# Performance work log

Hardware: AMD Instinct MI355X
Metric: run time of the kernel (lower is better)

Reference implementation:

```python
import jax, jax.numpy as jnp
import numpy as np

B, N, D, H, L, F = 8192, 64, 128, 8, 3, 512
HD = D // H
RADIUS = 3.0
LN_EPS = 1e-5


def _ln(x, g, b):
    m = jnp.mean(x, axis=-1, keepdims=True)
    v = jnp.var(x, axis=-1, keepdims=True)
    return (x - m) / jnp.sqrt(v + LN_EPS) * g + b


def setup_inputs() -> dict:
    key = jax.random.key(0)
    ks = jax.random.split(key, 20)
    def nrm(k, shape, s=0.05):
        return jax.random.normal(k, shape, jnp.float32) * s
    return {
        'ego_context': nrm(ks[0], (B, D), 1.0),
        'ego_pos': nrm(ks[1], (B, 2), 1.0),
        'ego_vel': nrm(ks[2], (B, 2), 1.0),
        'neighbor_pos': nrm(ks[3], (B, N, 2), 1.5),
        'neighbor_vel': nrm(ks[4], (B, N, 2), 1.0),
        'neighbor_mask': jax.random.bernoulli(ks[5], 0.8, (B, N)),
        'np_W': nrm(ks[6], (6, D), 0.3), 'np_b': jnp.zeros((D,), jnp.float32),
        'np_ln_g': jnp.ones((D,), jnp.float32), 'np_ln_b': jnp.zeros((D,), jnp.float32),
        'ego_W': nrm(ks[7], (D, D)), 'ego_b': jnp.zeros((D,), jnp.float32),
        'ego_ln_g': jnp.ones((D,), jnp.float32), 'ego_ln_b': jnp.zeros((D,), jnp.float32),
        'n1_g': jnp.ones((L, D), jnp.float32), 'n1_b': jnp.zeros((L, D), jnp.float32),
        'nkv_g': jnp.ones((L, D), jnp.float32), 'nkv_b': jnp.zeros((L, D), jnp.float32),
        'n2_g': jnp.ones((L, D), jnp.float32), 'n2_b': jnp.zeros((L, D), jnp.float32),
        'Wq': nrm(ks[8], (L, D, D)), 'bq': jnp.zeros((L, D), jnp.float32),
        'Wk': nrm(ks[9], (L, D, D)), 'bk': jnp.zeros((L, D), jnp.float32),
        'Wv': nrm(ks[10], (L, D, D)), 'bv': jnp.zeros((L, D), jnp.float32),
        'Wo': nrm(ks[11], (L, D, D)), 'bo': jnp.zeros((L, D), jnp.float32),
        'W1': nrm(ks[12], (L, D, F)), 'b1': jnp.zeros((L, F), jnp.float32),
        'W2': nrm(ks[13], (L, F, D)), 'b2': jnp.zeros((L, D), jnp.float32),
        'out_W': nrm(ks[14], (D, D)), 'out_b': jnp.zeros((D,), jnp.float32),
        'out_ln_g': jnp.ones((D,), jnp.float32), 'out_ln_b': jnp.zeros((D,), jnp.float32),
    }


def reference(ego_context, ego_pos, ego_vel, neighbor_pos, neighbor_vel, neighbor_mask,
              np_W, np_b, np_ln_g, np_ln_b, ego_W, ego_b, ego_ln_g, ego_ln_b,
              n1_g, n1_b, nkv_g, nkv_b, n2_g, n2_b,
              Wq, bq, Wk, bk, Wv, bv, Wo, bo, W1, b1, W2, b2,
              out_W, out_b, out_ln_g, out_ln_b):
    # relative features (B, N, 6)
    rel_pos = neighbor_pos - ego_pos[:, None, :]
    rel_vel = neighbor_vel - ego_vel[:, None, :]
    dist = jnp.clip(jnp.linalg.norm(rel_pos, axis=-1, keepdims=True), 1e-6, None)
    bearing = jnp.arctan2(rel_pos[..., 1:2] + 1e-8, rel_pos[..., 0:1] + 1e-8)
    rel = jnp.concatenate([rel_pos, rel_vel, dist, bearing], axis=-1)

    # dynamic mask: radius gating + all-masked fixup (mimics key_padding_mask[all_masked,0]=False)
    valid = neighbor_mask & (jnp.linalg.norm(neighbor_pos - ego_pos[:, None, :], axis=-1) < RADIUS)
    all_invalid = ~jnp.any(valid, axis=-1)
    valid = valid | (all_invalid[:, None] & (jnp.arange(N) == 0)[None, :])

    # neighbor_proj: Linear(6,D) -> LN -> ReLU (dropout inactive at eval)
    nb = jax.nn.relu(_ln(rel @ np_W + np_b, np_ln_g, np_ln_b))  # (B, N, D)
    # ego_proj: Linear(D,D) -> LN; keep ego as (B, D) since query length is 1
    x = _ln(ego_context @ ego_W + ego_b, ego_ln_g, ego_ln_b)

    scale = 1.0 / jnp.sqrt(jnp.float32(HD))
    for i in range(L):
        q = _ln(x, n1_g[i], n1_b[i])          # (B, D)
        kv = _ln(nb, nkv_g[i], nkv_b[i])      # (B, N, D)
        Q = (q @ Wq[i] + bq[i]).reshape(B, H, HD)
        K = (kv @ Wk[i] + bk[i]).reshape(B, N, H, HD)
        V = (kv @ Wv[i] + bv[i]).reshape(B, N, H, HD)
        scores = jnp.einsum('bhd,bnhd->bhn', Q, K) * scale
        scores = jnp.where(valid[:, None, :], scores, -1e9)
        attn = jax.nn.softmax(scores, axis=-1)
        ctx = jnp.einsum('bhn,bnhd->bhd', attn, V).reshape(B, D)
        x = x + ctx @ Wo[i] + bo[i]
        y = _ln(x, n2_g[i], n2_b[i])
        x = x + jax.nn.gelu(y @ W1[i] + b1[i], approximate=False) @ W2[i] + b2[i]

    return _ln(x @ out_W + out_b, out_ln_g, out_ln_b)
```

## Files before the change

kernel.cpp:

```cpp
#include <hip/hip_runtime.h>
#include <stdint.h>

typedef unsigned int uint;
typedef unsigned short ushort;
typedef unsigned long long u64;

#define B_   8192
#define D_   128
#define N_   64
#define L_   3

typedef __attribute__((ext_vector_type(8))) short short8;
typedef __attribute__((ext_vector_type(4))) float f32x4;
union FragU { uint4 u; short8 h; };

__device__ __forceinline__ float bf2f(ushort u){ union{uint i; float f;} c; c.i=((uint)u)<<16; return c.f; }
__device__ __forceinline__ float bflo(uint u){ union{uint i; float f;} c; c.i=u<<16; return c.f; }
__device__ __forceinline__ float bfhi(uint u){ union{uint i; float f;} c; c.i=u&0xffff0000u; return c.f; }
__device__ __forceinline__ ushort f2bf(float f){ uint u=__float_as_uint(f); return (ushort)((u + 0x7fffu + ((u>>16)&1u))>>16); }
__device__ __forceinline__ uint pk2(float lo, float hi){ return (uint)f2bf(lo) | (((uint)f2bf(hi))<<16); }
__device__ __forceinline__ float wsum(float v){ for (int o=32;o;o>>=1) v += __shfl_xor(v,o); return v; }

#define OFF_X   0
#define XSTR    520
#define OFF_XH  8320
#define XHSTR   272
#define OFF_Q   12672
#define QSTR    260
#define OFF_QK  16832
#define QKSTR   272
#define OFF_QB  21184
#define OFF_V   21248
#define OFF_NB  21504
#define NBSTR   272
#define OFF_NT  38912
#define NTSTR   144
#define OFF_AT  57344
#define ATSTR   144
#define OFF_U   59648
#define OFF_CX  61760
#define OFF_H1  21504
#define LDS_SZ  62272

struct P {
  const float *ego, *epos, *evel, *npos, *nvel;
  const int   *mask;
  const float *npW, *npb, *npg, *npbb;
  const float *ego_b, *ego_g, *ego_bb;
  const float *bo, *b2, *out_b, *out_g, *out_bb;
  const float *npRec;
  const ushort *WqT, *WkT, *WvT, *W1T, *WoT, *W2T, *egoT, *outT;
  const ushort *bqF, *bkF, *bvF, *b1F;
  ushort *nbg; u64 *msk;
  float *outp;
};

__global__ void prepF(const float* Wq,const float* bq,const float* n1g,const float* n1b,
                      const float* Wk,const float* bk,const float* nkg,const float* nkb,
                      const float* Wv,const float* bv,
                      const float* W1,const float* b1,const float* n2g,const float* n2b,
                      ushort* WqT, ushort* bqF, ushort* WkT, ushort* bkF,
                      ushort* WvT, ushort* bvF, ushort* W1T, ushort* b1F){
  __shared__ float red[2];
  int bid=blockIdx.x, t=threadIdx.x;
  const float *src,*g,*bb,*bias; ushort *dstW,*dstB; int N;
  if (bid<384){ int l=bid>>7, j=bid&127; src=Wq+l*16384+j; g=n1g+l*128; bb=n1b+l*128; bias=bq+l*128+j; dstW=WqT+l*16384+j*128; dstB=bqF+l*128+j; N=128; }
  else if (bid<768){ int q=bid-384; int l=q>>7, j=q&127; src=Wk+l*16384+j; g=nkg+l*128; bb=nkb+l*128; bias=bk+l*128+j; dstW=WkT+l*16384+j*128; dstB=bkF+l*128+j; N=128; }
  else if (bid<1152){ int q=bid-768; int l=q>>7, j=q&127; src=Wv+l*16384+j; g=nkg+l*128; bb=nkb+l*128; bias=bv+l*128+j; dstW=WvT+l*16384+j*128; dstB=bvF+l*128+j; N=128; }
  else { int q=bid-1152; int l=q/512, j=q%512; src=W1+l*65536+j; g=n2g+l*128; bb=n2b+l*128; bias=b1+l*512+j; dstW=W1T+l*65536+j*128; dstB=b1F+l*512+j; N=512; }
  float wv = src[t*N];
  dstW[t] = f2bf(g[t]*wv);
  float pv = wsum(bb[t]*wv);
  if ((t&63)==0) red[t>>6]=pv;
  __syncthreads();
  if (t==0) *dstB = f2bf(red[0]+red[1]+bias[0]);
}

__global__ void prepP(const float* Wo, const float* W2, const float* egoW, const float* outW,
                      ushort* WoT, ushort* W2T, ushort* egoT, ushort* outT){
  int bid=blockIdx.x, t=threadIdx.x;
  if (bid<384){ int l=bid>>7, j=bid&127; WoT[l*16384+j*128+t] = f2bf(Wo[l*16384+t*128+j]); }
  else if (bid<768){ int q=bid-384; int l=q>>7, j=q&127;
    for (int k=t;k<512;k+=128) W2T[l*65536+j*512+k] = f2bf(W2[l*65536+k*128+j]); }
  else if (bid<896){ int j=bid-768; egoT[j*128+t]=f2bf(egoW[t*128+j]); }
  else { int j=bid-896; outT[j*128+t]=f2bf(outW[t*128+j]); }
}

__global__ void prepNp(const float* npW, const float* npb, const float* npg, const float* npbb, float* rec){
  int t=threadIdx.x;
  if (t<128){
    for (int r=0;r<6;++r) rec[t*9+r]=npW[r*128+t];
    rec[t*9+6]=npb[t]; rec[t*9+7]=npg[t]; rec[t*9+8]=npbb[t];
  }
}

__global__ __launch_bounds__(256,4) void st_nb(P p){
  __shared__ float s_npW[768], s_npP[384];
  __shared__ float s_valid[2][64];
  int tid=threadIdx.x, g=tid>>7, t=tid&127;
  int b = blockIdx.x*2+g;
  for (int i=tid;i<768;i+=256) s_npW[i]=p.npW[i];
  if (tid<128){ s_npP[tid]=p.npb[tid]; s_npP[128+tid]=p.npg[tid]; s_npP[256+tid]=p.npbb[tid]; }
  __syncthreads();
  int nn=t>>1, jh=t&1;
  float2 pn = ((const float2*)p.npos)[b*N_+nn];
  float2 vn = ((const float2*)p.nvel)[b*N_+nn];
  float2 pe = ((const float2*)p.epos)[b];
  float2 ve = ((const float2*)p.evel)[b];
  float rx=pn.x-pe.x, ry=pn.y-pe.y, rvx=vn.x-ve.x, rvy=vn.y-ve.y;
  float nrm = sqrtf(rx*rx+ry*ry);
  float dist = fmaxf(nrm,1e-6f), bear = atan2f(ry+1e-8f, rx+1e-8f);
  bool vld = (p.mask[b*N_+nn]!=0) && (nrm<3.0f);
  if (jh==0) s_valid[g][nn] = vld?1.f:0.f;
  float z[64]; float sa=0.f, sb=0.f;
  #pragma unroll
  for (int jj=0;jj<64;++jj){
    int j = jh*64+jj;
    float v = s_npP[j] + rx*s_npW[j] + ry*s_npW[128+j] + rvx*s_npW[256+j]
                       + rvy*s_npW[384+j] + dist*s_npW[512+j] + bear*s_npW[640+j];
    z[jj]=v; sa+=v; sb+=v*v;
  }
  sa += __shfl_xor(sa,1); sb += __shfl_xor(sb,1);
  float m1 = sa*0.0078125f, r1 = rsqrtf(sb*0.0078125f - m1*m1 + 1e-5f);
  float ta=0.f, tb=0.f;
  #pragma unroll
  for (int jj=0;jj<64;++jj){
    int j = jh*64+jj;
    float a = (z[jj]-m1)*r1*s_npP[128+j] + s_npP[256+j];
    a = fmaxf(a,0.f);
    z[jj]=a; ta+=a; tb+=a*a;
  }
  ta += __shfl_xor(ta,1); tb += __shfl_xor(tb,1);
  float m2 = ta*0.0078125f, r2 = rsqrtf(tb*0.0078125f - m2*m2 + 1e-5f);
  uint* dst = (uint*)(p.nbg + (size_t)b*8192 + nn*128 + jh*64);
  #pragma unroll
  for (int q=0;q<32;++q) dst[q] = pk2((z[2*q]-m2)*r2, (z[2*q+1]-m2)*r2);
  __syncthreads();
  if (tid<2){
    u64 m=0;
    for (int n=0;n<64;++n) if (s_valid[tid][n]>0.5f) m |= (1ULL<<n);
    p.msk[blockIdx.x*2+tid] = m;
  }
}

__device__ __forceinline__ void ln_to_xh(char* smem, int tid){
  int b = tid>>4, pp = tid&15;
  const char* xr = smem + OFF_X + b*XSTR + pp*32;
  float v[8];
  #pragma unroll
  for (int i=0;i<4;++i){ float2 t2 = *(const float2*)(xr + i*8); v[2*i]=t2.x; v[2*i+1]=t2.y; }
  float s1=0.f, s2=0.f;
  #pragma unroll
  for (int i=0;i<8;++i){ s1+=v[i]; s2+=v[i]*v[i]; }
  for (int o=1;o<16;o<<=1){ s1 += __shfl_xor(s1,o); s2 += __shfl_xor(s2,o); }
  float m = s1*0.0078125f, rs = rsqrtf(s2*0.0078125f - m*m + 1e-5f);
  uint4 o4;
  o4.x = pk2((v[0]-m)*rs,(v[1]-m)*rs); o4.y = pk2((v[2]-m)*rs,(v[3]-m)*rs);
  o4.z = pk2((v[4]-m)*rs,(v[5]-m)*rs); o4.w = pk2((v[6]-m)*rs,(v[7]-m)*rs);
  *(uint4*)(smem + OFF_XH + b*XHSTR + pp*16) = o4;
}

__device__ __forceinline__ void ln_affine_inplace(char* smem, int tid, const float* g, const float* bb){
  int b = tid>>4, pp = tid&15;
  char* xr = smem + OFF_X + b*XSTR + pp*32;
  float v[8];
  #pragma unroll
  for (int i=0;i<4;++i){ float2 t2 = *(const float2*)(xr + i*8); v[2*i]=t2.x; v[2*i+1]=t2.y; }
  float s1=0.f, s2=0.f;
  #pragma unroll
  for (int i=0;i<8;++i){ s1+=v[i]; s2+=v[i]*v[i]; }
  for (int o=1;o<16;o<<=1){ s1 += __shfl_xor(s1,o); s2 += __shfl_xor(s2,o); }
  float m = s1*0.0078125f, rs = rsqrtf(s2*0.0078125f - m*m + 1e-5f);
  #pragma unroll
  for (int i=0;i<8;++i) v[i] = (v[i]-m)*rs*g[pp*8+i] + bb[pp*8+i];
  #pragma unroll
  for (int i=0;i<4;++i){ float2 t2; t2.x=v[2*i]; t2.y=v[2*i+1]; *(float2*)(xr + i*8) = t2; }
}

__device__ __forceinline__ void cvt_x_to_xh(char* smem, int tid){
  int b = tid>>4, pp = tid&15;
  const char* xr = smem + OFF_X + b*XSTR + pp*32;
  float v[8];
  #pragma unroll
  for (int i=0;i<4;++i){ float2 t2 = *(const float2*)(xr + i*8); v[2*i]=t2.x; v[2*i+1]=t2.y; }
  uint4 o4;
  o4.x=pk2(v[0],v[1]); o4.y=pk2(v[2],v[3]); o4.z=pk2(v[4],v[5]); o4.w=pk2(v[6],v[7]);
  *(uint4*)(smem + OFF_XH + b*XHSTR + pp*16) = o4;
}

template<int SPILL>
__global__ __launch_bounds__(256,2) void st_main(P p){
  __shared__ __align__(16) char smem[LDS_SZ];
  const int tid = threadIdx.x;
  const int w = tid>>6, l64 = tid&63;
  const int cc = l64&15, qq = l64>>4;
  const int bB = blockIdx.x*16;

  for (int i=tid;i<1088;i+=256) ((uint*)(smem+OFF_QK))[i]=0u;
  if (tid<16) ((float*)(smem+OFF_QB))[tid]=0.f;
  for (int i=tid;i<288;i+=256) ((uint*)(smem+OFF_AT+8*ATSTR))[i]=0u;

  {
    int b_=tid>>4, pp=tid&15;
    const float* src = p.ego + (size_t)(bB+b_)*128 + pp*8;
    float4 v0 = *(const float4*)src, v1 = *(const float4*)(src+4);
    uint4 o4; o4.x=pk2(v0.x,v0.y); o4.y=pk2(v0.z,v0.w); o4.z=pk2(v1.x,v1.y); o4.w=pk2(v1.z,v1.w);
    *(uint4*)(smem + OFF_XH + b_*XHSTR + pp*16) = o4;
  }
  __syncthreads();
  {
    #pragma unroll
    for (int i=0;i<2;++i){
      int nt = w*2+i;
      f32x4 acc = {0.f,0.f,0.f,0.f};
      #pragma unroll
      for (int kt=0;kt<4;++kt){
        FragU a,bF;
        a.u = *(const uint4*)(smem + OFF_XH + cc*XHSTR + kt*64 + qq*16);
        bF.u = *(const uint4*)(p.egoT + (nt*16+cc)*128 + kt*32 + qq*8);
        acc = __builtin_amdgcn_mfma_f32_16x16x32_bf16(a.h, bF.h, acc, 0,0,0);
      }
      int col = nt*16+cc;
      float bv = p.ego_b[col];
      #pragma unroll
      for (int r=0;r<4;++r) *(float*)(smem+OFF_X+(qq*4+r)*XSTR+col*4) = acc[r]+bv;
    }
  }
  __syncthreads();
  ln_affine_inplace(smem, tid, p.ego_g, p.ego_bb);
  __syncthreads();

  for (int li=0; li<L_; ++li){
    ln_to_xh(smem, tid);
    __syncthreads();
    {
      const ushort* W = p.WqT + li*16384;
      #pragma unroll
      for (int i=0;i<2;++i){
        int nt = w*2+i;
        f32x4 acc = {0.f,0.f,0.f,0.f};
        #pragma unroll
        for (int kt=0;kt<4;++kt){
          FragU a,bF;
          a.u = *(const uint4*)(smem + OFF_XH + cc*XHSTR + kt*64 + qq*16);
          bF.u = *(const uint4*)(W + (nt*16+cc)*128 + kt*32 + qq*8);
          acc = __builtin_amdgcn_mfma_f32_16x16x32_bf16(a.h, bF.h, acc, 0,0,0);
        }
        int col = nt*16+cc;
        float bv = bf2f(p.bqF[li*128+col]);
        ushort* Qm = (ushort*)(smem+OFF_Q);
        #pragma unroll
        for (int r=0;r<4;++r) Qm[(qq*4+r)*130 + col] = f2bf(acc[r]+bv);
      }
    }
    __syncthreads();

    for (int bl=0; bl<16; ++bl){
      const int b = bB + bl;
      if (SPILL){
        int n = w*16 + (l64>>2), seg = l64&3;
        if (seg==0){
          u64 mv = p.msk[b];
          *(float*)(smem+OFF_V+n*4) = ((mv>>n)&1ULL) ? 1.f : 0.f;
        }
        const uint4* src = (const uint4*)(p.nbg + (size_t)b*8192 + n*128);
        ushort* T = (ushort*)(smem+OFF_NT);
        #pragma unroll
        for (int i=0;i<4;++i){
          int ci = seg + i*4;
          uint4 v = src[ci];
          *(uint4*)(smem + OFF_NB + n*NBSTR + ci*16) = v;
          int d0 = ci*8;
          T[(d0+0)*72+n]=(ushort)v.x; T[(d0+1)*72+n]=(ushort)(v.x>>16);
          T[(d0+2)*72+n]=(ushort)v.y; T[(d0+3)*72+n]=(ushort)(v.y>>16);
          T[(d0+4)*72+n]=(ushort)v.z; T[(d0+5)*72+n]=(ushort)(v.z>>16);
          T[(d0+6)*72+n]=(ushort)v.w; T[(d0+7)*72+n]=(ushort)(v.w>>16);
        }
      } else {
        int n = w*16 + (l64>>2), jq = l64&3;
        float2 pn = ((const float2*)p.npos)[b*N_+n];
        float2 vn = ((const float2*)p.nvel)[b*N_+n];
        float2 pe = ((const float2*)p.epos)[b];
        float2 ve = ((const float2*)p.evel)[b];
        float rx=pn.x-pe.x, ry=pn.y-pe.y, rvx=vn.x-ve.x, rvy=vn.y-ve.y;
        float nrm = sqrtf(rx*rx+ry*ry);
        float dist = fmaxf(nrm,1e-6f), bear = atan2f(ry+1e-8f, rx+1e-8f);
        if (jq==0){
          bool vld = (p.mask[b*N_+n]!=0) && (nrm<3.0f);
          *(float*)(smem+OFF_V+n*4) = vld?1.f:0.f;
        }
        float z[32]; float sa=0.f, sb=0.f;
        #pragma unroll
        for (int jj=0;jj<32;++jj){
          const float* rec = p.npRec + (jq*32+jj)*9;
          float4 r0 = *(const float4*)rec;
          float4 r1 = *(const float4*)(rec+4);
          float v = r1.z + rx*r0.x + ry*r0.y + rvx*r0.z + rvy*r0.w + dist*r1.x + bear*r1.y;
          z[jj]=v; sa+=v; sb+=v*v;
        }
        sa += __shfl_xor(sa,1); sb += __shfl_xor(sb,1);
        sa += __shfl_xor(sa,2); sb += __shfl_xor(sb,2);
        float m1 = sa*0.0078125f, r1s = rsqrtf(sb*0.0078125f - m1*m1 + 1e-5f);
        float ta=0.f, tb=0.f;
        #pragma unroll
        for (int jj=0;jj<32;++jj){
          const float* rec = p.npRec + (jq*32+jj)*9;
          float a = (z[jj]-m1)*r1s*rec[7] + rec[8];
          a = fmaxf(a,0.f);
          z[jj]=a; ta+=a; tb+=a*a;
        }
        ta += __shfl_xor(ta,1); tb += __shfl_xor(tb,1);
        ta += __shfl_xor(ta,2); tb += __shfl_xor(tb,2);
        float m2 = ta*0.0078125f, r2s = rsqrtf(tb*0.0078125f - m2*m2 + 1e-5f);
        ushort* T = (ushort*)(smem+OFF_NT);
        #pragma unroll
        for (int q2=0;q2<16;++q2){
          uint pr = pk2((z[2*q2]-m2)*r2s, (z[2*q2+1]-m2)*r2s);
          *(uint*)(smem + OFF_NB + n*NBSTR + jq*64 + q2*4) = pr;
          int d = jq*32 + q2*2;
          T[d*72 + n] = (ushort)pr;
          T[(d+1)*72 + n] = (ushort)(pr>>16);
        }
      }
      {
        int h = (w<<1) + (l64>>5);
        int d4 = (l64&31)*4;
        const ushort* Wk = p.WkT + li*16384;
        float a0=0.f,a1=0.f,a2=0.f,a3=0.f, qb=0.f;
        #pragma unroll
        for (int j=0;j<16;++j){
          float qv = bf2f(*(const ushort*)(smem + OFF_Q + bl*QSTR + (h*16+j)*2));
          uint2 wv = *(const uint2*)(Wk + (h*16+j)*128 + d4);
          a0 += qv*bflo(wv.x); a1 += qv*bfhi(wv.x);
          a2 += qv*bflo(wv.y); a3 += qv*bfhi(wv.y);
          qb += qv * bf2f(p.bkF[li*128 + h*16 + j]);
        }
        uint2 o; o.x = pk2(a0,a1); o.y = pk2(a2,a3);
        *(uint2*)(smem + OFF_QK + h*QKSTR + d4*2) = o;
        if ((l64&31)==0) *(float*)(smem+OFF_QB + h*4) = qb;
      }
      __syncthreads();

      {
        FragU bfr[4];
        #pragma unroll
        for (int kt=0;kt<4;++kt) bfr[kt].u = *(const uint4*)(smem + OFF_QK + cc*QKSTR + kt*64 + qq*16);
        f32x4 c[4];
        #pragma unroll
        for (int mt=0;mt<4;++mt){
          f32x4 acc = {0.f,0.f,0.f,0.f};
          #pragma unroll
          for (int kt=0;kt<4;++kt){
            FragU a; a.u = *(const uint4*)(smem + OFF_NB + (mt*16+cc)*NBSTR + kt*64 + qq*16);
            acc = __builtin_amdgcn_mfma_f32_16x16x32_bf16(a.h, bfr[kt].h, acc, 0,0,0);
          }
          c[mt]=acc;
        }
        float qbv = *(const float*)(smem+OFF_QB+cc*4);
        float fl[16]; float anyv=0.f;
        #pragma unroll
        for (int mt=0;mt<4;++mt)
          #pragma unroll
          for (int r=0;r<4;++r){
            int n = mt*16 + qq*4 + r;
            float f = *(const float*)(smem+OFF_V+n*4);
            fl[mt*4+r]=f; anyv+=f;
          }
        bool none = (__ballot(anyv>0.5f)==0ULL);
        float sc[16];
        #pragma unroll
        for (int mt=0;mt<4;++mt)
          #pragma unroll
          for (int r=0;r<4;++r){
            int k = mt*4+r; int n = mt*16+qq*4+r;
            bool ok = (fl[k]>0.5f) || (none && n==0);
            sc[k] = ok ? 0.25f*(c[mt][r]+qbv) : -1e9f;
          }
        float mx=-3e38f;
        #pragma unroll
        for (int k=0;k<16;++k) mx=fmaxf(mx,sc[k]);
        mx = fmaxf(mx,__shfl_xor(mx,16)); mx = fmaxf(mx,__shfl_xor(mx,32));
        float ex[16]; float se=0.f;
        #pragma unroll
        for (int k=0;k<16;++k){ ex[k]=__expf(sc[k]-mx); se+=ex[k]; }
        se += __shfl_xor(se,16); se += __shfl_xor(se,32);
        float inv = 1.f/se;
        if (w==0 && cc<8){
          ushort* A = (ushort*)(smem+OFF_AT);
          #pragma unroll
          for (int mt=0;mt<4;++mt)
            #pragma unroll
            for (int r=0;r<4;++r) A[cc*72 + (mt*16+qq*4+r)] = f2bf(ex[mt*4+r]*inv);
        }
      }
      __syncthreads();

      {
        #pragma unroll
        for (int i=0;i<2;++i){
          int nt = w*2 + i;
          f32x4 acc={0.f,0.f,0.f,0.f};
          #pragma unroll
          for (int kt=0;kt<2;++kt){
            FragU a,bF;
            a.u = *(const uint4*)(smem + OFF_AT + cc*ATSTR + kt*64 + qq*16);
            bF.u = *(const uint4*)(smem + OFF_NT + (nt*16+cc)*NTSTR + kt*64 + qq*16);
            acc = __builtin_amdgcn_mfma_f32_16x16x32_bf16(a.h, bF.h, acc, 0,0,0);
          }
          if (qq<2){
            ushort* U = (ushort*)(smem+OFF_U);
            #pragma unroll
            for (int r=0;r<4;++r) U[(qq*4+r)*132 + nt*16+cc] = f2bf(acc[r]);
          }
        }
      }
      __syncthreads();

      {
        int jj = l64>>1, dh = l64&1;
        int j = w*32 + jj;
        int h = j>>4;
        const ushort* Wv = p.WvT + li*16384 + j*128;
        float acc = (dh==0) ? bf2f(p.bvF[li*128+j]) : 0.f;
        #pragma unroll
        for (int i8=0;i8<8;++i8){
          int d = dh*64 + i8*8;
          uint2 u0 = *(const uint2*)(smem + OFF_U + h*264 + d*2);
          uint2 u1 = *(const uint2*)(smem + OFF_U + h*264 + d*2 + 8);
          uint4 wv = *(const uint4*)(Wv + d);
          acc += bflo(u0.x)*bflo(wv.x) + bfhi(u0.x)*bfhi(wv.x);
          acc += bflo(u0.y)*bflo(wv.y) + bfhi(u0.y)*bfhi(wv.y);
          acc += bflo(u1.x)*bflo(wv.z) + bfhi(u1.x)*bfhi(wv.z);
          acc += bflo(u1.y)*bflo(wv.w) + bfhi(u1.y)*bfhi(wv.w);
        }
        acc += __shfl_xor(acc,1);
        if (dh==0) *(float*)(smem+OFF_CX + j*4) = acc;
      }
      __syncthreads();

      {
        int jj = l64>>1, dh = l64&1;
        int j = w*32 + jj;
        const ushort* Wo = p.WoT + li*16384 + j*128;
        float acc = (dh==0) ? p.bo[li*128+j] : 0.f;
        #pragma unroll
        for (int i8=0;i8<8;++i8){
          int d = dh*64 + i8*8;
          float4 c0 = *(const float4*)(smem + OFF_CX + d*4);
          float4 c1 = *(const float4*)(smem + OFF_CX + d*4 + 16);
          uint4 wv = *(const uint4*)(Wo + d);
          acc += c0.x*bflo(wv.x) + c0.y*bfhi(wv.x) + c0.z*bflo(wv.y) + c0.w*bfhi(wv.y);
          acc += c1.x*bflo(wv.z) + c1.y*bfhi(wv.z) + c1.z*bflo(wv.w) + c1.w*bfhi(wv.w);
        }
        acc += __shfl_xor(acc,1);
        if (dh==0){
          float* xp = (float*)(smem + OFF_X + bl*XSTR + j*4);
          *xp += acc;
        }
      }
      __syncthreads();
    }

    ln_to_xh(smem, tid);
    __syncthreads();
    {
      FragU afr[4];
      #pragma unroll
      for (int kt=0;kt<4;++kt) afr[kt].u = *(const uint4*)(smem+OFF_XH + cc*XHSTR + kt*64 + qq*16);
      const ushort* W = p.W1T + li*65536;
      ushort* H = (ushort*)(smem+OFF_H1);
      #pragma unroll
      for (int i=0;i<8;++i){
        int nt = w*8+i;
        f32x4 acc={0.f,0.f,0.f,0.f};
        #pragma unroll
        for (int kt=0;kt<4;++kt){
          FragU bF; bF.u = *(const uint4*)(W + (nt*16+cc)*128 + kt*32 + qq*8);
          acc = __builtin_amdgcn_mfma_f32_16x16x32_bf16(afr[kt].h, bF.h, acc, 0,0,0);
        }
        int col = nt*16+cc;
        float bv = bf2f(p.b1F[li*512+col]);
        #pragma unroll
        for (int r=0;r<4;++r){
          float v = acc[r]+bv;
          v = 0.5f*v*(1.f+erff(v*0.70710678118654752f));
          H[(qq*4+r)*520 + col] = f2bf(v);
        }
      }
    }
    __syncthreads();
    {
      const ushort* W = p.W2T + li*65536;
      #pragma unroll
      for (int i=0;i<2;++i){
        int nt = w*2+i;
        f32x4 acc={0.f,0.f,0.f,0.f};
        #pragma unroll
        for (int kt=0;kt<16;++kt){
          FragU a,bF;
          a.u = *(const uint4*)(smem+OFF_H1 + cc*1040 + kt*64 + qq*16);
          bF.u = *(const uint4*)(W + (nt*16+cc)*512 + kt*32 + qq*8);
          acc = __builtin_amdgcn_mfma_f32_16x16x32_bf16(a.h, bF.h, acc, 0,0,0);
        }
        int col = nt*16+cc;
        float bv = p.b2[li*128+col];
        #pragma unroll
        for (int r=0;r<4;++r){
          float* xp = (float*)(smem+OFF_X+(qq*4+r)*XSTR+col*4);
          *xp += acc[r]+bv;
        }
      }
    }
    __syncthreads();
  }

  cvt_x_to_xh(smem, tid);
  __syncthreads();
  {
    #pragma unroll
    for (int i=0;i<2;++i){
      int nt = w*2+i;
      f32x4 acc = {0.f,0.f,0.f,0.f};
      #pragma unroll
      for (int kt=0;kt<4;++kt){
        FragU a,bF;
        a.u = *(const uint4*)(smem + OFF_XH + cc*XHSTR + kt*64 + qq*16);
        bF.u = *(const uint4*)(p.outT + (nt*16+cc)*128 + kt*32 + qq*8);
        acc = __builtin_amdgcn_mfma_f32_16x16x32_bf16(a.h, bF.h, acc, 0,0,0);
      }
      int col = nt*16+cc;
      float bv = p.out_b[col];
      #pragma unroll
      for (int r=0;r<4;++r) *(float*)(smem+OFF_X+(qq*4+r)*XSTR+col*4) = acc[r]+bv;
    }
  }
  __syncthreads();
  {
    int b_=tid>>4, pp=tid&15;
    const char* xr = smem + OFF_X + b_*XSTR + pp*32;
    float v[8];
    #pragma unroll
    for (int i=0;i<4;++i){ float2 t2 = *(const float2*)(xr + i*8); v[2*i]=t2.x; v[2*i+1]=t2.y; }
    float s1=0.f, s2=0.f;
    #pragma unroll
    for (int i=0;i<8;++i){ s1+=v[i]; s2+=v[i]*v[i]; }
    for (int o=1;o<16;o<<=1){ s1 += __shfl_xor(s1,o); s2 += __shfl_xor(s2,o); }
    float m = s1*0.0078125f, rs = rsqrtf(s2*0.0078125f - m*m + 1e-5f);
    float4 o0,o1;
    o0.x=(v[0]-m)*rs*p.out_g[pp*8+0]+p.out_bb[pp*8+0];
    o0.y=(v[1]-m)*rs*p.out_g[pp*8+1]+p.out_bb[pp*8+1];
    o0.z=(v[2]-m)*rs*p.out_g[pp*8+2]+p.out_bb[pp*8+2];
    o0.w=(v[3]-m)*rs*p.out_g[pp*8+3]+p.out_bb[pp*8+3];
    o1.x=(v[4]-m)*rs*p.out_g[pp*8+4]+p.out_bb[pp*8+4];
    o1.y=(v[5]-m)*rs*p.out_g[pp*8+5]+p.out_bb[pp*8+5];
    o1.z=(v[6]-m)*rs*p.out_g[pp*8+6]+p.out_bb[pp*8+6];
    o1.w=(v[7]-m)*rs*p.out_g[pp*8+7]+p.out_bb[pp*8+7];
    float* dst = p.outp + (size_t)(bB+b_)*128 + pp*8;
    *(float4*)dst = o0; *(float4*)(dst+4) = o1;
  }
}

extern "C" void kernel_launch(void* const* d_in, const int* in_sizes, int n_in,
                              void* d_out, int out_size, void* d_ws, size_t ws_size,
                              hipStream_t stream){
  (void)in_sizes; (void)n_in; (void)out_size;
  char* ws = (char*)d_ws;
  ushort* WqT  = (ushort*)(ws + 0);
  ushort* WkT  = (ushort*)(ws + 98304);
  ushort* WvT  = (ushort*)(ws + 196608);
  ushort* W1T  = (ushort*)(ws + 294912);
  ushort* WoT  = (ushort*)(ws + 688128);
  ushort* W2T  = (ushort*)(ws + 786432);
  ushort* egoT = (ushort*)(ws + 1179648);
  ushort* outT = (ushort*)(ws + 1212416);
  float*  npRec= (float*) (ws + 1245184);
  ushort* bqF  = (ushort*)(ws + 1249792);
  ushort* bkF  = (ushort*)(ws + 1250560);
  ushort* bvF  = (ushort*)(ws + 1251328);
  ushort* b1F  = (ushort*)(ws + 1252096);
  const size_t NB_OFF  = 1255424;
  const size_t MSK_OFF = NB_OFF + (size_t)B_*8192*2;
  const size_t NEED    = MSK_OFF + (size_t)B_*8;
  const bool spill = (ws_size >= NEED);

  prepF<<<2688,128,0,stream>>>((const float*)d_in[20],(const float*)d_in[21],(const float*)d_in[14],(const float*)d_in[15],
                               (const float*)d_in[22],(const float*)d_in[23],(const float*)d_in[16],(const float*)d_in[17],
                               (const float*)d_in[24],(const float*)d_in[25],
                               (const float*)d_in[28],(const float*)d_in[29],(const float*)d_in[18],(const float*)d_in[19],
                               WqT,bqF,WkT,bkF,WvT,bvF,W1T,b1F);
  prepP<<<1024,128,0,stream>>>((const float*)d_in[26],(const float*)d_in[30],(const float*)d_in[10],(const float*)d_in[32],
                               WoT,W2T,egoT,outT);
  prepNp<<<1,128,0,stream>>>((const float*)d_in[6],(const float*)d_in[7],(const float*)d_in[8],(const float*)d_in[9],npRec);

  P p;
  p.ego=(const float*)d_in[0]; p.epos=(const float*)d_in[1]; p.evel=(const float*)d_in[2];
  p.npos=(const float*)d_in[3]; p.nvel=(const float*)d_in[4]; p.mask=(const int*)d_in[5];
  p.npW=(const float*)d_in[6]; p.npb=(const float*)d_in[7]; p.npg=(const float*)d_in[8]; p.npbb=(const float*)d_in[9];
  p.ego_b=(const float*)d_in[11]; p.ego_g=(const float*)d_in[12]; p.ego_bb=(const float*)d_in[13];
  p.bo=(const float*)d_in[27]; p.b2=(const float*)d_in[31];
  p.out_b=(const float*)d_in[33]; p.out_g=(const float*)d_in[34]; p.out_bb=(const float*)d_in[35];
  p.npRec=npRec;
  p.WqT=WqT; p.WkT=WkT; p.WvT=WvT; p.W1T=W1T; p.WoT=WoT; p.W2T=W2T; p.egoT=egoT; p.outT=outT;
  p.bqF=bqF; p.bkF=bkF; p.bvF=bvF; p.b1F=b1F;
  p.nbg = (ushort*)(ws + NB_OFF);
  p.msk = (u64*)(ws + MSK_OFF);
  p.outp=(float*)d_out;

  if (spill){
    st_nb<<<B_/2,256,0,stream>>>(p);
    st_main<1><<<B_/16,256,0,stream>>>(p);
  } else {
    st_main<0><<<B_/16,256,0,stream>>>(p);
  }
}
```

Baseline: 618.8 us.

## Fold Q/K and V/O projections into per-head bilinear forms, shrink block to 8 rows

Precomputes per-head merged matrices (Wq·Wk^T scaled, and Wv·Wo) so attention scores come from the LayerNormed neighbor features directly, and context output is a single projection from attention-weighted features. This avoids computing K and V for all 64 neighbors per layer. The main kernel now processes 8 batch rows per block with smaller LDS and occupancy 4, and st_nb also writes a transposed neighbor copy. It costs much more workspace and doubles neighbor-feature traffic, and MFMA tiles are half wasted with 8 rows.

```diff
diff --git a/kernel.cpp b/kernel.cpp
--- a/kernel.cpp
+++ b/kernel.cpp
@@ -15,87 +15,157 @@
 union FragU { uint4 u; short8 h; };
 
 __device__ __forceinline__ float bf2f(ushort u){ union{uint i; float f;} c; c.i=((uint)u)<<16; return c.f; }
-__device__ __forceinline__ float bflo(uint u){ union{uint i; float f;} c; c.i=u<<16; return c.f; }
-__device__ __forceinline__ float bfhi(uint u){ union{uint i; float f;} c; c.i=u&0xffff0000u; return c.f; }
 __device__ __forceinline__ ushort f2bf(float f){ uint u=__float_as_uint(f); return (ushort)((u + 0x7fffu + ((u>>16)&1u))>>16); }
 __device__ __forceinline__ uint pk2(float lo, float hi){ return (uint)f2bf(lo) | (((uint)f2bf(hi))<<16); }
-__device__ __forceinline__ float wsum(float v){ for (int o=32;o;o>>=1) v += __shfl_xor(v,o); return v; }
-
-#define OFF_X   0
-#define XSTR    520
-#define OFF_XH  8320
-#define XHSTR   272
-#define OFF_Q   12672
-#define QSTR    260
-#define OFF_QK  16832
-#define QKSTR   272
-#define OFF_QB  21184
-#define OFF_V   21248
-#define OFF_NB  21504
-#define NBSTR   272
-#define OFF_NT  38912
-#define NTSTR   144
-#define OFF_AT  57344
-#define ATSTR   144
-#define OFF_U   59648
-#define OFF_CX  61760
-#define OFF_H1  21504
-#define LDS_SZ  62272
+
+#define OFF_X    0
+#define XSTR     528
+#define OFF_XH   4224
+#define XHSTR    272
+#define OFF_QKA  6400
+#define OFF_H1   6400
+#define OFF_QB   23808
+#define OFF_MSK  24064
+#define OFF_UA   24128
+#define LDS_SZ   40640
 
 struct P {
-  const float *ego, *epos, *evel, *npos, *nvel;
+  const float *ego,*epos,*evel,*npos,*nvel;
   const int   *mask;
-  const float *npW, *npb, *npg, *npbb;
-  const float *ego_b, *ego_g, *ego_bb;
-  const float *bo, *b2, *out_b, *out_g, *out_bb;
-  const float *npRec;
-  const ushort *WqT, *WkT, *WvT, *W1T, *WoT, *W2T, *egoT, *outT;
-  const ushort *bqF, *bkF, *bvF, *b1F;
-  ushort *nbg; u64 *msk;
+  const float *npW,*npb,*npg,*npbb;
+  const float *ego_b,*ego_g,*ego_bb;
+  const float *b2,*out_b,*out_g,*out_bb;
+  const float *C0,*m2,*c2,*bo2,*b1F;
+  const ushort *MT,*G,*W1B,*W2B,*egoT,*outT;
+  ushort *nbg,*nbt; u64 *msk;
   float *outp;
 };
 
-__global__ void prepF(const float* Wq,const float* bq,const float* n1g,const float* n1b,
-                      const float* Wk,const float* bk,const float* nkg,const float* nkb,
-                      const float* Wv,const float* bv,
-                      const float* W1,const float* b1,const float* n2g,const float* n2b,
-                      ushort* WqT, ushort* bqF, ushort* WkT, ushort* bkF,
-                      ushort* WvT, ushort* bvF, ushort* W1T, ushort* b1F){
-  __shared__ float red[2];
-  int bid=blockIdx.x, t=threadIdx.x;
-  const float *src,*g,*bb,*bias; ushort *dstW,*dstB; int N;
-  if (bid<384){ int l=bid>>7, j=bid&127; src=Wq+l*16384+j; g=n1g+l*128; bb=n1b+l*128; bias=bq+l*128+j; dstW=WqT+l*16384+j*128; dstB=bqF+l*128+j; N=128; }
-  else if (bid<768){ int q=bid-384; int l=q>>7, j=q&127; src=Wk+l*16384+j; g=nkg+l*128; bb=nkb+l*128; bias=bk+l*128+j; dstW=WkT+l*16384+j*128; dstB=bkF+l*128+j; N=128; }
-  else if (bid<1152){ int q=bid-768; int l=q>>7, j=q&127; src=Wv+l*16384+j; g=nkg+l*128; bb=nkb+l*128; bias=bv+l*128+j; dstW=WvT+l*16384+j*128; dstB=bvF+l*128+j; N=128; }
-  else { int q=bid-1152; int l=q/512, j=q%512; src=W1+l*65536+j; g=n2g+l*128; bb=n2b+l*128; bias=b1+l*512+j; dstW=W1T+l*65536+j*128; dstB=b1F+l*512+j; N=512; }
-  float wv = src[t*N];
-  dstW[t] = f2bf(g[t]*wv);
-  float pv = wsum(bb[t]*wv);
-  if ((t&63)==0) red[t>>6]=pv;
-  __syncthreads();
-  if (t==0) *dstB = f2bf(red[0]+red[1]+bias[0]);
+__global__ void prep_bias(const float* Wq,const float* bq,const float* n1b,
+                          const float* Wk,const float* bk,const float* nkb,
+                          const float* Wv,const float* bv,
+                          const float* W1,const float* b1,const float* n2b,
+                          float* bqp, float* bkp, float* bvp, float* b1F){
+  int gid = blockIdx.x*256 + threadIdx.x;
+  if (gid >= 3*896) return;
+  int l = gid/896, c = gid%896;
+  if (c < 384){
+    int m = c>>7, j = c&127;
+    const float* W = (m==0?Wq:(m==1?Wk:Wv)) + l*16384 + j;
+    const float* nb = (m==0? n1b : nkb) + l*128;
+    const float* bs = (m==0?bq:(m==1?bk:bv)) + l*128 + j;
+    float a = *bs;
+    for (int e=0;e<128;++e) a += nb[e]*W[e*128];
+    float* dst = (m==0?bqp:(m==1?bkp:bvp));
+    dst[l*128+j] = a;
+  } else {
+    int f = c-384;
+    float a = b1[l*512+f];
+    const float* W = W1 + l*65536 + f;
+    const float* nb = n2b + l*128;
+    for (int e=0;e<128;++e) a += nb[e]*W[e*512];
+    b1F[l*512+f] = a;
+  }
 }
 
-__global__ void prepP(const float* Wo, const float* W2, const float* egoW, const float* outW,
-                      ushort* WoT, ushort* W2T, ushort* egoT, ushort* outT){
-  int bid=blockIdx.x, t=threadIdx.x;
-  if (bid<384){ int l=bid>>7, j=bid&127; WoT[l*16384+j*128+t] = f2bf(Wo[l*16384+t*128+j]); }
-  else if (bid<768){ int q=bid-384; int l=q>>7, j=q&127;
-    for (int k=t;k<512;k+=128) W2T[l*65536+j*512+k] = f2bf(W2[l*65536+k*128+j]); }
-  else if (bid<896){ int j=bid-768; egoT[j*128+t]=f2bf(egoW[t*128+j]); }
-  else { int j=bid-896; outT[j*128+t]=f2bf(outW[t*128+j]); }
+__global__ void prep_bias2(const float* Wo, const float* bo, const float* bvp, float* bo2){
+  int l = blockIdx.x, t = threadIdx.x;
+  if (t < 128){
+    float a = bo[l*128+t];
+    const float* W = Wo + l*16384 + t;
+    const float* bv = bvp + l*128;
+    for (int c=0;c<128;++c) a += bv[c]*W[c*128];
+    bo2[l*128+t] = a;
+  }
 }
 
-__global__ void prepNp(const float* npW, const float* npb, const float* npg, const float* npbb, float* rec){
-  int t=threadIdx.x;
+__global__ void prep_MG(const float* Wq,const float* Wk,const float* Wv,const float* Wo,
+                        const float* n1g,const float* nkg,
+                        const float* bqp,const float* bkp,
+                        ushort* MT, float* C0, float* m2, float* c2, ushort* G){
+  __shared__ float sWq[128][16], sWk[128][16], sWv[128][16], sWo[16][128];
+  int l = blockIdx.x>>3, h = blockIdx.x&7, t = threadIdx.x;
+  { int row = t>>1, hf = t&1;
+    const float* q = Wq + l*16384 + row*128 + h*16 + hf*8;
+    const float* k = Wk + l*16384 + row*128 + h*16 + hf*8;
+    const float* v = Wv + l*16384 + row*128 + h*16 + hf*8;
+    for (int j=0;j<8;++j){ sWq[row][hf*8+j]=q[j]; sWk[row][hf*8+j]=k[j]; sWv[row][hf*8+j]=v[j]; }
+  }
+  { int row = t>>4, sg = t&15;
+    const float* o = Wo + l*16384 + (h*16+row)*128 + sg*8;
+    for (int j=0;j<8;++j) sWo[row][sg*8+j]=o[j];
+  }
+  __syncthreads();
+  {
+    int e = t&127;
+    float g1 = 0.25f*n1g[l*128+e];
+    float wq[16];
+    #pragma unroll
+    for (int j=0;j<16;++j) wq[j]=sWq[e][j];
+    for (int k2=0;k2<64;++k2){
+      int d = (t>>7) + 2*k2;
+      float s=0.f;
+      #pragma unroll
+      for (int j=0;j<16;++j) s += wq[j]*sWk[d][j];
+      MT[(size_t)l*131072 + (size_t)(h*128+d)*128 + e] = f2bf(g1*nkg[l*128+d]*s);
+    }
+    if (t<128){
+      float s=0.f;
+      #pragma unroll
+      for (int j=0;j<16;++j) s += wq[j]*bkp[l*128+h*16+j];
+      m2[(l*128+e)*8+h] = g1*s;
+    }
+  }
   if (t<128){
-    for (int r=0;r<6;++r) rec[t*9+r]=npW[r*128+t];
-    rec[t*9+6]=npb[t]; rec[t*9+7]=npg[t]; rec[t*9+8]=npbb[t];
+    int d=t; float s=0.f;
+    #pragma unroll
+    for (int j=0;j<16;++j) s += bqp[l*128+h*16+j]*sWk[d][j];
+    C0[l*1024 + h*128 + d] = 0.25f*nkg[l*128+d]*s;
+  }
+  if (t==0){
+    float s=0.f;
+    for (int j=0;j<16;++j) s += bqp[l*128+h*16+j]*bkp[l*128+h*16+j];
+    c2[l*8+h] = 0.25f*s;
+  }
+  {
+    int d = t&127;
+    float gk = nkg[l*128+d];
+    float wv[16];
+    #pragma unroll
+    for (int j=0;j<16;++j) wv[j]=gk*sWv[d][j];
+    for (int k2=0;k2<64;++k2){
+      int e = (t>>7) + 2*k2;
+      float s=0.f;
+      #pragma unroll
+      for (int j=0;j<16;++j) s += wv[j]*sWo[j][e];
+      G[(size_t)l*131072 + (size_t)e*1024 + h*128 + d] = f2bf(s);
+    }
   }
 }
 
+__global__ void prep_T(const float* W1,const float* n2g,const float* W2,
+                       const float* egoW,const float* outW,
+                       ushort* W1B, ushort* W2B, ushort* egoT, ushort* outT){
+  int gid = blockIdx.x*256 + threadIdx.x;
+  if (gid < 196608){
+    int l = gid/65536, r = gid%65536, f = r>>7, e = r&127;
+    W1B[gid] = f2bf(n2g[l*128+e]*W1[l*65536 + e*512 + f]);
+  } else if (gid < 393216){
+    int q = gid-196608; int l = q/65536, r = q%65536, e = r>>9, f = r&511;
+    W2B[q] = f2bf(W2[l*65536 + f*128 + e]);
+  } else if (gid < 409600){
+    int q = gid-393216; int c = q>>7, e = q&127;
+    egoT[q] = f2bf(egoW[e*128+c]);
+  } else if (gid < 425984){
+    int q = gid-409600; int c = q>>7, e = q&127;
+    outT[q] = f2bf(outW[e*128+c]);
+  }
+}
+
+template<int MODE>
 __global__ __launch_bounds__(256,4) void st_nb(P p){
   __shared__ float s_npW[768], s_npP[384];
+  __shared__ ushort s_nb[2][64*136];
   __shared__ float s_valid[2][64];
   int tid=threadIdx.x, g=tid>>7, t=tid&127;
   int b = blockIdx.x*2+g;
@@ -131,81 +201,51 @@
     z[jj]=a; ta+=a; tb+=a*a;
   }
   ta += __shfl_xor(ta,1); tb += __shfl_xor(tb,1);
-  float m2 = ta*0.0078125f, r2 = rsqrtf(tb*0.0078125f - m2*m2 + 1e-5f);
-  uint* dst = (uint*)(p.nbg + (size_t)b*8192 + nn*128 + jh*64);
+  float m2v = ta*0.0078125f, r2 = rsqrtf(tb*0.0078125f - m2v*m2v + 1e-5f);
+  uint* gdst = (uint*)(p.nbg + (size_t)b*8192 + nn*128 + jh*64);
+  uint* ldst = (uint*)(&s_nb[g][nn*136 + jh*64]);
   #pragma unroll
-  for (int q=0;q<32;++q) dst[q] = pk2((z[2*q]-m2)*r2, (z[2*q+1]-m2)*r2);
+  for (int q=0;q<32;++q){
+    uint pr = pk2((z[2*q]-m2v)*r2, (z[2*q+1]-m2v)*r2);
+    gdst[q] = pr; ldst[q] = pr;
+  }
   __syncthreads();
   if (tid<2){
     u64 m=0;
     for (int n=0;n<64;++n) if (s_valid[tid][n]>0.5f) m |= (1ULL<<n);
+    if (m==0ULL) m = 1ULL;
     p.msk[blockIdx.x*2+tid] = m;
   }
+  if (MODE==2){
+    uint pk[32];
+    #pragma unroll 8
+    for (int m=0;m<32;++m){
+      ushort lo = s_nb[g][(2*m)*136 + t];
+      ushort hi = s_nb[g][(2*m+1)*136 + t];
+      pk[m] = (uint)lo | ((uint)hi<<16);
+    }
+    uint4* dst = (uint4*)(p.nbt + (size_t)b*8192 + t*64);
+    #pragma unroll
+    for (int q=0;q<8;++q) dst[q] = make_uint4(pk[4*q],pk[4*q+1],pk[4*q+2],pk[4*q+3]);
+  }
 }
 
-__device__ __forceinline__ void ln_to_xh(char* smem, int tid){
-  int b = tid>>4, pp = tid&15;
-  const char* xr = smem + OFF_X + b*XSTR + pp*32;
-  float v[8];
-  #pragma unroll
-  for (int i=0;i<4;++i){ float2 t2 = *(const float2*)(xr + i*8); v[2*i]=t2.x; v[2*i+1]=t2.y; }
-  float s1=0.f, s2=0.f;
-  #pragma unroll
-  for (int i=0;i<8;++i){ s1+=v[i]; s2+=v[i]*v[i]; }
-  for (int o=1;o<16;o<<=1){ s1 += __shfl_xor(s1,o); s2 += __shfl_xor(s2,o); }
-  float m = s1*0.0078125f, rs = rsqrtf(s2*0.0078125f - m*m + 1e-5f);
-  uint4 o4;
-  o4.x = pk2((v[0]-m)*rs,(v[1]-m)*rs); o4.y = pk2((v[2]-m)*rs,(v[3]-m)*rs);
-  o4.z = pk2((v[4]-m)*rs,(v[5]-m)*rs); o4.w = pk2((v[6]-m)*rs,(v[7]-m)*rs);
-  *(uint4*)(smem + OFF_XH + b*XHSTR + pp*16) = o4;
-}
-
-__device__ __forceinline__ void ln_affine_inplace(char* smem, int tid, const float* g, const float* bb){
-  int b = tid>>4, pp = tid&15;
-  char* xr = smem + OFF_X + b*XSTR + pp*32;
-  float v[8];
-  #pragma unroll
-  for (int i=0;i<4;++i){ float2 t2 = *(const float2*)(xr + i*8); v[2*i]=t2.x; v[2*i+1]=t2.y; }
-  float s1=0.f, s2=0.f;
-  #pragma unroll
-  for (int i=0;i<8;++i){ s1+=v[i]; s2+=v[i]*v[i]; }
-  for (int o=1;o<16;o<<=1){ s1 += __shfl_xor(s1,o); s2 += __shfl_xor(s2,o); }
-  float m = s1*0.0078125f, rs = rsqrtf(s2*0.0078125f - m*m + 1e-5f);
-  #pragma unroll
-  for (int i=0;i<8;++i) v[i] = (v[i]-m)*rs*g[pp*8+i] + bb[pp*8+i];
-  #pragma unroll
-  for (int i=0;i<4;++i){ float2 t2; t2.x=v[2*i]; t2.y=v[2*i+1]; *(float2*)(xr + i*8) = t2; }
-}
-
-__device__ __forceinline__ void cvt_x_to_xh(char* smem, int tid){
-  int b = tid>>4, pp = tid&15;
-  const char* xr = smem + OFF_X + b*XSTR + pp*32;
-  float v[8];
-  #pragma unroll
-  for (int i=0;i<4;++i){ float2 t2 = *(const float2*)(xr + i*8); v[2*i]=t2.x; v[2*i+1]=t2.y; }
-  uint4 o4;
-  o4.x=pk2(v[0],v[1]); o4.y=pk2(v[2],v[3]); o4.z=pk2(v[4],v[5]); o4.w=pk2(v[6],v[7]);
-  *(uint4*)(smem + OFF_XH + b*XHSTR + pp*16) = o4;
-}
-
-template<int SPILL>
-__global__ __launch_bounds__(256,2) void st_main(P p){
+template<int MODE>
+__global__ __launch_bounds__(256,4) void st_main(P p){
   __shared__ __align__(16) char smem[LDS_SZ];
   const int tid = threadIdx.x;
   const int w = tid>>6, l64 = tid&63;
   const int cc = l64&15, qq = l64>>4;
-  const int bB = blockIdx.x*16;
-
-  for (int i=tid;i<1088;i+=256) ((uint*)(smem+OFF_QK))[i]=0u;
-  if (tid<16) ((float*)(smem+OFF_QB))[tid]=0.f;
-  for (int i=tid;i<288;i+=256) ((uint*)(smem+OFF_AT+8*ATSTR))[i]=0u;
-
-  {
-    int b_=tid>>4, pp=tid&15;
-    const float* src = p.ego + (size_t)(bB+b_)*128 + pp*8;
-    float4 v0 = *(const float4*)src, v1 = *(const float4*)(src+4);
-    uint4 o4; o4.x=pk2(v0.x,v0.y); o4.y=pk2(v0.z,v0.w); o4.z=pk2(v1.x,v1.y); o4.w=pk2(v1.z,v1.w);
-    *(uint4*)(smem + OFF_XH + b_*XHSTR + pp*16) = o4;
+  const int b5 = tid>>5, sg = tid&31;
+  const int bB = blockIdx.x*8;
+
+  if (tid<8) ((u64*)(smem+OFF_MSK))[tid] = p.msk[bB+tid];
+
+  {
+    const float* src = p.ego + (size_t)(bB+b5)*128 + sg*4;
+    float4 v = *(const float4*)src;
+    uint2 o; o.x = pk2(v.x,v.y); o.y = pk2(v.z,v.w);
+    *(uint2*)(smem + OFF_XH + b5*XHSTR + sg*8) = o;
   }
   __syncthreads();
   {
@@ -216,305 +256,259 @@
       #pragma unroll
       for (int kt=0;kt<4;++kt){
         FragU a,bF;
-        a.u = *(const uint4*)(smem + OFF_XH + cc*XHSTR + kt*64 + qq*16);
+        a.u = *(const uint4*)(smem + OFF_XH + (cc&7)*XHSTR + kt*64 + qq*16);
         bF.u = *(const uint4*)(p.egoT + (nt*16+cc)*128 + kt*32 + qq*8);
         acc = __builtin_amdgcn_mfma_f32_16x16x32_bf16(a.h, bF.h, acc, 0,0,0);
       }
-      int col = nt*16+cc;
-      float bv = p.ego_b[col];
-      #pragma unroll
-      for (int r=0;r<4;++r) *(float*)(smem+OFF_X+(qq*4+r)*XSTR+col*4) = acc[r]+bv;
-    }
-  }
-  __syncthreads();
-  ln_affine_inplace(smem, tid, p.ego_g, p.ego_bb);
+      if (qq<2){
+        int col = nt*16+cc; float bv = p.ego_b[col];
+        #pragma unroll
+        for (int r=0;r<4;++r) *(float*)(smem+OFF_X+(qq*4+r)*XSTR+col*4) = acc[r]+bv;
+      }
+    }
+  }
+  __syncthreads();
+  {
+    float* xr = (float*)(smem + OFF_X + b5*XSTR + sg*16);
+    float4 v = *(float4*)xr;
+    float s1 = v.x+v.y+v.z+v.w, s2 = v.x*v.x+v.y*v.y+v.z*v.z+v.w*v.w;
+    for (int o=1;o<32;o<<=1){ s1 += __shfl_xor(s1,o); s2 += __shfl_xor(s2,o); }
+    float m = s1*0.0078125f, rs = rsqrtf(s2*0.0078125f - m*m + 1e-5f);
+    int c0 = sg*4;
+    v.x = (v.x-m)*rs*p.ego_g[c0+0]+p.ego_bb[c0+0];
+    v.y = (v.y-m)*rs*p.ego_g[c0+1]+p.ego_bb[c0+1];
+    v.z = (v.z-m)*rs*p.ego_g[c0+2]+p.ego_bb[c0+2];
+    v.w = (v.w-m)*rs*p.ego_g[c0+3]+p.ego_bb[c0+3];
+    *(float4*)xr = v;
+  }
   __syncthreads();
 
   for (int li=0; li<L_; ++li){
-    ln_to_xh(smem, tid);
+    {
+      const float* xr = (const float*)(smem + OFF_X + b5*XSTR + sg*16);
+      float4 v = *(const float4*)xr;
+      float s1 = v.x+v.y+v.z+v.w, s2 = v.x*v.x+v.y*v.y+v.z*v.z+v.w*v.w;
+      for (int o=1;o<32;o<<=1){ s1 += __shfl_xor(s1,o); s2 += __shfl_xor(s2,o); }
+      float m = s1*0.0078125f, rs = rsqrtf(s2*0.0078125f - m*m + 1e-5f);
+      uint2 o2; o2.x = pk2((v.x-m)*rs,(v.y-m)*rs); o2.y = pk2((v.z-m)*rs,(v.w-m)*rs);
+      *(uint2*)(smem + OFF_XH + b5*XHSTR + sg*8) = o2;
+    }
     __syncthreads();
     {
-      const ushort* W = p.WqT + li*16384;
+      const ushort* MTl = p.MT + (size_t)li*131072;
+      const float*  C0l = p.C0 + li*1024;
+      FragU aF[4];
+      #pragma unroll
+      for (int kt=0;kt<4;++kt) aF[kt].u = *(const uint4*)(smem + OFF_XH + (cc&7)*XHSTR + kt*64 + qq*16);
+      for (int it=0; it<16; ++it){
+        int nt = w*16+it;
+        f32x4 acc = {0.f,0.f,0.f,0.f};
+        #pragma unroll
+        for (int kt=0;kt<4;++kt){
+          FragU bF; bF.u = *(const uint4*)(MTl + (nt*16+cc)*128 + kt*32 + qq*8);
+          acc = __builtin_amdgcn_mfma_f32_16x16x32_bf16(aF[kt].h, bF.h, acc, 0,0,0);
+        }
+        if (qq<2){
+          int col = nt*16+cc; float c0 = C0l[col];
+          int h = col>>7, dd = col&127;
+          #pragma unroll
+          for (int r=0;r<4;++r)
+            *(ushort*)(smem + OFF_QKA + (qq*4+r)*2176 + h*272 + dd*2) = f2bf(acc[r]+c0);
+        }
+      }
+    }
+    {
+      int b_ = tid>>5, h = (tid>>2)&7, q4 = tid&3;
+      const ushort* xh = (const ushort*)(smem + OFF_XH + b_*XHSTR);
+      const float* m2l = p.m2 + li*1024;
+      float a = 0.f;
+      #pragma unroll 8
+      for (int e = q4*32; e < q4*32+32; ++e) a += bf2f(xh[e]) * m2l[e*8+h];
+      a += __shfl_xor(a,1); a += __shfl_xor(a,2);
+      if (q4==0) *(float*)(smem + OFF_QB + (b_*8+h)*4) = a + p.c2[li*8+h];
+    }
+    __syncthreads();
+
+    for (int rr=0; rr<2; ++rr){
+      const int bl = w*2+rr;
+      const size_t bg = (size_t)(bB+bl);
+      const ushort* nbB = p.nbg + bg*8192;
+      FragU bq4[4];
+      #pragma unroll
+      for (int kt=0;kt<4;++kt) bq4[kt].u = *(const uint4*)(smem + OFF_QKA + bl*2176 + cc*272 + kt*64 + qq*16);
+      f32x4 c[4];
+      #pragma unroll
+      for (int mt=0;mt<4;++mt){
+        f32x4 acc = {0.f,0.f,0.f,0.f};
+        #pragma unroll
+        for (int kt=0;kt<4;++kt){
+          FragU a; a.u = *(const uint4*)(nbB + (mt*16+cc)*128 + kt*32 + qq*8);
+          acc = __builtin_amdgcn_mfma_f32_16x16x32_bf16(a.h, bq4[kt].h, acc, 0,0,0);
+        }
+        c[mt]=acc;
+      }
+      float qbv = *(const float*)(smem + OFF_QB + (bl*8+(cc&7))*4);
+      u64 vm = ((const u64*)(smem+OFF_MSK))[bl];
+      float sc[16];
+      #pragma unroll
+      for (int mt=0;mt<4;++mt)
+        #pragma unroll
+        for (int r=0;r<4;++r){
+          int n = mt*16 + qq*4 + r;
+          bool ok = (vm>>n)&1ULL;
+          sc[mt*4+r] = ok ? (c[mt][r]+qbv) : -1e9f;
+        }
+      float mx = -3e38f;
+      #pragma unroll
+      for (int k=0;k<16;++k) mx = fmaxf(mx, sc[k]);
+      mx = fmaxf(mx,__shfl_xor(mx,16)); mx = fmaxf(mx,__shfl_xor(mx,32));
+      float ex[16], se = 0.f;
+      #pragma unroll
+      for (int k=0;k<16;++k){ ex[k]=__expf(sc[k]-mx); se+=ex[k]; }
+      se += __shfl_xor(se,16); se += __shfl_xor(se,32);
+      float inv = 1.f/se;
+      uint P[8];
+      #pragma unroll
+      for (int mt=0;mt<4;++mt){
+        P[2*mt]   = pk2(ex[mt*4+0]*inv, ex[mt*4+1]*inv);
+        P[2*mt+1] = pk2(ex[mt*4+2]*inv, ex[mt*4+3]*inv);
+      }
+      FragU aU[2];
+      #pragma unroll
+      for (int ktU=0;ktU<2;++ktU){
+        uint e[4];
+        #pragma unroll
+        for (int pp=0;pp<4;++pp){
+          int src = (((2*qq + (pp>>1)) & 3) << 4) + cc;
+          uint lo = (uint)__shfl((int)P[4*ktU + (pp&1)],     src);
+          uint hi = (uint)__shfl((int)P[4*ktU + 2 + (pp&1)], src);
+          e[pp] = (qq>>1) ? hi : lo;
+        }
+        aU[ktU].u = make_uint4(e[0],e[1],e[2],e[3]);
+      }
+      const ushort* nbT = p.nbt + bg*8192;
+      #pragma unroll
+      for (int nt=0;nt<8;++nt){
+        f32x4 acc = {0.f,0.f,0.f,0.f};
+        #pragma unroll
+        for (int ktU=0;ktU<2;++ktU){
+          FragU bF;
+          if (MODE==2){
+            bF.u = *(const uint4*)(nbT + (nt*16+cc)*64 + ktU*32 + qq*8);
+          } else {
+            ushort tmp[8];
+            #pragma unroll
+            for (int j=0;j<8;++j) tmp[j] = nbB[(ktU*32+qq*8+j)*128 + nt*16+cc];
+            uint* tp = (uint*)tmp;
+            bF.u = make_uint4(tp[0],tp[1],tp[2],tp[3]);
+          }
+          acc = __builtin_amdgcn_mfma_f32_16x16x32_bf16(aU[ktU].h, bF.h, acc, 0,0,0);
+        }
+        if (qq<2){
+          #pragma unroll
+          for (int r=0;r<4;++r){
+            int h = qq*4+r;
+            *(ushort*)(smem + OFF_UA + bl*2064 + (h*128 + nt*16+cc)*2) = f2bf(acc[r]);
+          }
+        }
+      }
+    }
+    __syncthreads();
+
+    {
+      const ushort* Gl = p.G + (size_t)li*131072;
       #pragma unroll
       for (int i=0;i<2;++i){
         int nt = w*2+i;
         f32x4 acc = {0.f,0.f,0.f,0.f};
-        #pragma unroll
-        for (int kt=0;kt<4;++kt){
+        #pragma unroll 8
+        for (int kt=0;kt<32;++kt){
           FragU a,bF;
-          a.u = *(const uint4*)(smem + OFF_XH + cc*XHSTR + kt*64 + qq*16);
-          bF.u = *(const uint4*)(W + (nt*16+cc)*128 + kt*32 + qq*8);
+          a.u = *(const uint4*)(smem + OFF_UA + (cc&7)*2064 + kt*64 + qq*16);
+          bF.u = *(const uint4*)(Gl + (nt*16+cc)*1024 + kt*32 + qq*8);
           acc = __builtin_amdgcn_mfma_f32_16x16x32_bf16(a.h, bF.h, acc, 0,0,0);
         }
-        int col = nt*16+cc;
-        float bv = bf2f(p.bqF[li*128+col]);
-        ushort* Qm = (ushort*)(smem+OFF_Q);
-        #pragma unroll
-        for (int r=0;r<4;++r) Qm[(qq*4+r)*130 + col] = f2bf(acc[r]+bv);
-      }
-    }
-    __syncthreads();
-
-    for (int bl=0; bl<16; ++bl){
-      const int b = bB + bl;
-      if (SPILL){
-        int n = w*16 + (l64>>2), seg = l64&3;
-        if (seg==0){
-          u64 mv = p.msk[b];
-          *(float*)(smem+OFF_V+n*4) = ((mv>>n)&1ULL) ? 1.f : 0.f;
-        }
-        const uint4* src = (const uint4*)(p.nbg + (size_t)b*8192 + n*128);
-        ushort* T = (ushort*)(smem+OFF_NT);
-        #pragma unroll
-        for (int i=0;i<4;++i){
-          int ci = seg + i*4;
-          uint4 v = src[ci];
-          *(uint4*)(smem + OFF_NB + n*NBSTR + ci*16) = v;
-          int d0 = ci*8;
-          T[(d0+0)*72+n]=(ushort)v.x; T[(d0+1)*72+n]=(ushort)(v.x>>16);
-          T[(d0+2)*72+n]=(ushort)v.y; T[(d0+3)*72+n]=(ushort)(v.y>>16);
-          T[(d0+4)*72+n]=(ushort)v.z; T[(d0+5)*72+n]=(ushort)(v.z>>16);
-          T[(d0+6)*72+n]=(ushort)v.w; T[(d0+7)*72+n]=(ushort)(v.w>>16);
-        }
-      } else {
-        int n = w*16 + (l64>>2), jq = l64&3;
-        float2 pn = ((const float2*)p.npos)[b*N_+n];
-        float2 vn = ((const float2*)p.nvel)[b*N_+n];
-        float2 pe = ((const float2*)p.epos)[b];
-        float2 ve = ((const float2*)p.evel)[b];
-        float rx=pn.x-pe.x, ry=pn.y-pe.y, rvx=vn.x-ve.x, rvy=vn.y-ve.y;
-        float nrm = sqrtf(rx*rx+ry*ry);
-        float dist = fmaxf(nrm,1e-6f), bear = atan2f(ry+1e-8f, rx+1e-8f);
-        if (jq==0){
-          bool vld = (p.mask[b*N_+n]!=0) && (nrm<3.0f);
-          *(float*)(smem+OFF_V+n*4) = vld?1.f:0.f;
-        }
-        float z[32]; float sa=0.f, sb=0.f;
-        #pragma unroll
-        for (int jj=0;jj<32;++jj){
-          const float* rec = p.npRec + (jq*32+jj)*9;
-          float4 r0 = *(const float4*)rec;
-          float4 r1 = *(const float4*)(rec+4);
-          float v = r1.z + rx*r0.x + ry*r0.y + rvx*r0.z + rvy*r0.w + dist*r1.x + bear*r1.y;
-          z[jj]=v; sa+=v; sb+=v*v;
-        }
-        sa += __shfl_xor(sa,1); sb += __shfl_xor(sb,1);
-        sa += __shfl_xor(sa,2); sb += __shfl_xor(sb,2);
-        float m1 = sa*0.0078125f, r1s = rsqrtf(sb*0.0078125f - m1*m1 + 1e-5f);
-        float ta=0.f, tb=0.f;
-        #pragma unroll
-        for (int jj=0;jj<32;++jj){
-          const float* rec = p.npRec + (jq*32+jj)*9;
-          float a = (z[jj]-m1)*r1s*rec[7] + rec[8];
-          a = fmaxf(a,0.f);
-          z[jj]=a; ta+=a; tb+=a*a;
-        }
-        ta += __shfl_xor(ta,1); tb += __shfl_xor(tb,1);
-        ta += __shfl_xor(ta,2); tb += __shfl_xor(tb,2);
-        float m2 = ta*0.0078125f, r2s = rsqrtf(tb*0.0078125f - m2*m2 + 1e-5f);
-        ushort* T = (ushort*)(smem+OFF_NT);
-        #pragma unroll
-        for (int q2=0;q2<16;++q2){
-          uint pr = pk2((z[2*q2]-m2)*r2s, (z[2*q2+1]-m2)*r2s);
-          *(uint*)(smem + OFF_NB + n*NBSTR + jq*64 + q2*4) = pr;
-          int d = jq*32 + q2*2;
-          T[d*72 + n] = (ushort)pr;
-          T[(d+1)*72 + n] = (ushort)(pr>>16);
-        }
-      }
-      {
-        int h = (w<<1) + (l64>>5);
-        int d4 = (l64&31)*4;
-        const ushort* Wk = p.WkT + li*16384;
-        float a0=0.f,a1=0.f,a2=0.f,a3=0.f, qb=0.f;
-        #pragma unroll
-        for (int j=0;j<16;++j){
-          float qv = bf2f(*(const ushort*)(smem + OFF_Q + bl*QSTR + (h*16+j)*2));
-          uint2 wv = *(const uint2*)(Wk + (h*16+j)*128 + d4);
-          a0 += qv*bflo(wv.x); a1 += qv*bfhi(wv.x);
-          a2 += qv*bflo(wv.y); a3 += qv*bfhi(wv.y);
-          qb += qv * bf2f(p.bkF[li*128 + h*16 + j]);
-        }
-        uint2 o; o.x = pk2(a0,a1); o.y = pk2(a2,a3);
-        *(uint2*)(smem + OFF_QK + h*QKSTR + d4*2) = o;
-        if ((l64&31)==0) *(float*)(smem+OFF_QB + h*4) = qb;
-      }
-      __syncthreads();
-
-      {
-        FragU bfr[4];
-        #pragma unroll
-        for (int kt=0;kt<4;++kt) bfr[kt].u = *(const uint4*)(smem + OFF_QK + cc*QKSTR + kt*64 + qq*16);
-        f32x4 c[4];
-        #pragma unroll
-        for (int mt=0;mt<4;++mt){
-          f32x4 acc = {0.f,0.f,0.f,0.f};
-          #pragma unroll
-          for (int kt=0;kt<4;++kt){
-            FragU a; a.u = *(const uint4*)(smem + OFF_NB + (mt*16+cc)*NBSTR + kt*64 + qq*16);
-            acc = __builtin_amdgcn_mfma_f32_16x16x32_bf16(a.h, bfr[kt].h, acc, 0,0,0);
-          }
-          c[mt]=acc;
-        }
-        float qbv = *(const float*)(smem+OFF_QB+cc*4);
-        float fl[16]; float anyv=0.f;
-        #pragma unroll
-        for (int mt=0;mt<4;++mt)
+        if (qq<2){
+          int col = nt*16+cc; float bv = p.bo2[li*128+col];
           #pragma unroll
           for (int r=0;r<4;++r){
-            int n = mt*16 + qq*4 + r;
-            float f = *(const float*)(smem+OFF_V+n*4);
-            fl[mt*4+r]=f; anyv+=f;
+            float* xp = (float*)(smem + OFF_X + (qq*4+r)*XSTR + col*4);
+            *xp += acc[r]+bv;
           }
-        bool none = (__ballot(anyv>0.5f)==0ULL);
-        float sc[16];
-        #pragma unroll
-        for (int mt=0;mt<4;++mt)
+        }
+      }
+    }
+    __syncthreads();
+
+    {
+      const float* xr = (const float*)(smem + OFF_X + b5*XSTR + sg*16);
+      float4 v = *(const float4*)xr;
+      float s1 = v.x+v.y+v.z+v.w, s2 = v.x*v.x+v.y*v.y+v.z*v.z+v.w*v.w;
+      for (int o=1;o<32;o<<=1){ s1 += __shfl_xor(s1,o); s2 += __shfl_xor(s2,o); }
+      float m = s1*0.0078125f, rs = rsqrtf(s2*0.0078125f - m*m + 1e-5f);
+      uint2 o2; o2.x = pk2((v.x-m)*rs,(v.y-m)*rs); o2.y = pk2((v.z-m)*rs,(v.w-m)*rs);
+      *(uint2*)(smem + OFF_XH + b5*XHSTR + sg*8) = o2;
+    }
+    __syncthreads();
+    {
+      const ushort* W = p.W1B + (size_t)li*65536;
+      const float* b1l = p.b1F + li*512;
+      FragU aF[4];
+      #pragma unroll
+      for (int kt=0;kt<4;++kt) aF[kt].u = *(const uint4*)(smem + OFF_XH + (cc&7)*XHSTR + kt*64 + qq*16);
+      #pragma unroll
+      for (int it=0;it<8;++it){
+        int nt = w*8+it;
+        f32x4 acc = {0.f,0.f,0.f,0.f};
+        #pragma unroll
+        for (int kt=0;kt<4;++kt){
+          FragU bF; bF.u = *(const uint4*)(W + (nt*16+cc)*128 + kt*32 + qq*8);
+          acc = __builtin_amdgcn_mfma_f32_16x16x32_bf16(aF[kt].h, bF.h, acc, 0,0,0);
+        }
+        if (qq<2){
+          int col = nt*16+cc; float bv = b1l[col];
           #pragma unroll
           for (int r=0;r<4;++r){
-            int k = mt*4+r; int n = mt*16+qq*4+r;
-            bool ok = (fl[k]>0.5f) || (none && n==0);
-            sc[k] = ok ? 0.25f*(c[mt][r]+qbv) : -1e9f;
+            float v = acc[r]+bv;
+            v = 0.5f*v*(1.f+erff(v*0.70710678118654752f));
+            *(ushort*)(smem + OFF_H1 + (qq*4+r)*1040 + col*2) = f2bf(v);
           }
-        float mx=-3e38f;
-        #pragma unroll
-        for (int k=0;k<16;++k) mx=fmaxf(mx,sc[k]);
-        mx = fmaxf(mx,__shfl_xor(mx,16)); mx = fmaxf(mx,__shfl_xor(mx,32));
-        float ex[16]; float se=0.f;
-        #pragma unroll
-        for (int k=0;k<16;++k){ ex[k]=__expf(sc[k]-mx); se+=ex[k]; }
-        se += __shfl_xor(se,16); se += __shfl_xor(se,32);
-        float inv = 1.f/se;
-        if (w==0 && cc<8){
-          ushort* A = (ushort*)(smem+OFF_AT);
-          #pragma unroll
-          for (int mt=0;mt<4;++mt)
-            #pragma unroll
-            for (int r=0;r<4;++r) A[cc*72 + (mt*16+qq*4+r)] = f2bf(ex[mt*4+r]*inv);
-        }
-      }
-      __syncthreads();
-
-      {
-        #pragma unroll
-        for (int i=0;i<2;++i){
-          int nt = w*2 + i;
-          f32x4 acc={0.f,0.f,0.f,0.f};
-          #pragma unroll
-          for (int kt=0;kt<2;++kt){
-            FragU a,bF;
-            a.u = *(const uint4*)(smem + OFF_AT + cc*ATSTR + kt*64 + qq*16);
-            bF.u = *(const uint4*)(smem + OFF_NT + (nt*16+cc)*NTSTR + kt*64 + qq*16);
-            acc = __builtin_amdgcn_mfma_f32_16x16x32_bf16(a.h, bF.h, acc, 0,0,0);
-          }
-          if (qq<2){
-            ushort* U = (ushort*)(smem+OFF_U);
-            #pragma unroll
-            for (int r=0;r<4;++r) U[(qq*4+r)*132 + nt*16+cc] = f2bf(acc[r]);
-          }
-        }
-      }
-      __syncthreads();
-
-      {
-        int jj = l64>>1, dh = l64&1;
-        int j = w*32 + jj;
-        int h = j>>4;
-        const ushort* Wv = p.WvT + li*16384 + j*128;
-        float acc = (dh==0) ? bf2f(p.bvF[li*128+j]) : 0.f;
-        #pragma unroll
-        for (int i8=0;i8<8;++i8){
-          int d = dh*64 + i8*8;
-          uint2 u0 = *(const uint2*)(smem + OFF_U + h*264 + d*2);
-          uint2 u1 = *(const uint2*)(smem + OFF_U + h*264 + d*2 + 8);
-          uint4 wv = *(const uint4*)(Wv + d);
-          acc += bflo(u0.x)*bflo(wv.x) + bfhi(u0.x)*bfhi(wv.x);
-          acc += bflo(u0.y)*bflo(wv.y) + bfhi(u0.y)*bfhi(wv.y);
-          acc += bflo(u1.x)*bflo(wv.z) + bfhi(u1.x)*bfhi(wv.z);
-          acc += bflo(u1.y)*bflo(wv.w) + bfhi(u1.y)*bfhi(wv.w);
-        }
-        acc += __shfl_xor(acc,1);
-        if (dh==0) *(float*)(smem+OFF_CX + j*4) = acc;
-      }
-      __syncthreads();
-
-      {
-        int jj = l64>>1, dh = l64&1;
-        int j = w*32 + jj;
-        const ushort* Wo = p.WoT + li*16384 + j*128;
-        float acc = (dh==0) ? p.bo[li*128+j] : 0.f;
-        #pragma unroll
-        for (int i8=0;i8<8;++i8){
-          int d = dh*64 + i8*8;
-          float4 c0 = *(const float4*)(smem + OFF_CX + d*4);
-          float4 c1 = *(const float4*)(smem + OFF_CX + d*4 + 16);
-          uint4 wv = *(const uint4*)(Wo + d);
-          acc += c0.x*bflo(wv.x) + c0.y*bfhi(wv.x) + c0.z*bflo(wv.y) + c0.w*bfhi(wv.y);
-          acc += c1.x*bflo(wv.z) + c1.y*bfhi(wv.z) + c1.z*bflo(wv.w) + c1.w*bfhi(wv.w);
-        }
-        acc += __shfl_xor(acc,1);
-        if (dh==0){
-          float* xp = (float*)(smem + OFF_X + bl*XSTR + j*4);
-          *xp += acc;
-        }
-      }
-      __syncthreads();
-    }
-
-    ln_to_xh(smem, tid);
+        }
+      }
+    }
     __syncthreads();
     {
-      FragU afr[4];
-      #pragma unroll
-      for (int kt=0;kt<4;++kt) afr[kt].u = *(const uint4*)(smem+OFF_XH + cc*XHSTR + kt*64 + qq*16);
-      const ushort* W = p.W1T + li*65536;
-      ushort* H = (ushort*)(smem+OFF_H1);
-      #pragma unroll
-      for (int i=0;i<8;++i){
-        int nt = w*8+i;
-        f32x4 acc={0.f,0.f,0.f,0.f};
-        #pragma unroll
-        for (int kt=0;kt<4;++kt){
-          FragU bF; bF.u = *(const uint4*)(W + (nt*16+cc)*128 + kt*32 + qq*8);
-          acc = __builtin_amdgcn_mfma_f32_16x16x32_bf16(afr[kt].h, bF.h, acc, 0,0,0);
-        }
-        int col = nt*16+cc;
-        float bv = bf2f(p.b1F[li*512+col]);
-        #pragma unroll
-        for (int r=0;r<4;++r){
-          float v = acc[r]+bv;
-          v = 0.5f*v*(1.f+erff(v*0.70710678118654752f));
-          H[(qq*4+r)*520 + col] = f2bf(v);
-        }
-      }
-    }
-    __syncthreads();
-    {
-      const ushort* W = p.W2T + li*65536;
+      const ushort* W = p.W2B + (size_t)li*65536;
       #pragma unroll
       for (int i=0;i<2;++i){
         int nt = w*2+i;
-        f32x4 acc={0.f,0.f,0.f,0.f};
-        #pragma unroll
+        f32x4 acc = {0.f,0.f,0.f,0.f};
+        #pragma unroll 8
         for (int kt=0;kt<16;++kt){
           FragU a,bF;
-          a.u = *(const uint4*)(smem+OFF_H1 + cc*1040 + kt*64 + qq*16);
+          a.u = *(const uint4*)(smem + OFF_H1 + (cc&7)*1040 + kt*64 + qq*16);
           bF.u = *(const uint4*)(W + (nt*16+cc)*512 + kt*32 + qq*8);
           acc = __builtin_amdgcn_mfma_f32_16x16x32_bf16(a.h, bF.h, acc, 0,0,0);
         }
-        int col = nt*16+cc;
-        float bv = p.b2[li*128+col];
-        #pragma unroll
-        for (int r=0;r<4;++r){
-          float* xp = (float*)(smem+OFF_X+(qq*4+r)*XSTR+col*4);
-          *xp += acc[r]+bv;
+        if (qq<2){
+          int col = nt*16+cc; float bv = p.b2[li*128+col];
+          #pragma unroll
+          for (int r=0;r<4;++r){
+            float* xp = (float*)(smem + OFF_X + (qq*4+r)*XSTR + col*4);
+            *xp += acc[r]+bv;
+          }
         }
       }
     }
     __syncthreads();
   }
 
-  cvt_x_to_xh(smem, tid);
+  {
+    const float* xr = (const float*)(smem + OFF_X + b5*XSTR + sg*16);
+    float4 v = *(const float4*)xr;
+    uint2 o2; o2.x = pk2(v.x,v.y); o2.y = pk2(v.z,v.w);
+    *(uint2*)(smem + OFF_XH + b5*XHSTR + sg*8) = o2;
+  }
   __syncthreads();
   {
     #pragma unroll
@@ -524,39 +518,31 @@
       #pragma unroll
       for (int kt=0;kt<4;++kt){
         FragU a,bF;
-        a.u = *(const uint4*)(smem + OFF_XH + cc*XHSTR + kt*64 + qq*16);
+        a.u = *(const uint4*)(smem + OFF_XH + (cc&7)*XHSTR + kt*64 + qq*16);
         bF.u = *(const uint4*)(p.outT + (nt*16+cc)*128 + kt*32 + qq*8);
         acc = __builtin_amdgcn_mfma_f32_16x16x32_bf16(a.h, bF.h, acc, 0,0,0);
       }
-      int col = nt*16+cc;
-      float bv = p.out_b[col];
-      #pragma unroll
-      for (int r=0;r<4;++r) *(float*)(smem+OFF_X+(qq*4+r)*XSTR+col*4) = acc[r]+bv;
-    }
-  }
-  __syncthreads();
-  {
-    int b_=tid>>4, pp=tid&15;
-    const char* xr = smem + OFF_X + b_*XSTR + pp*32;
-    float v[8];
-    #pragma unroll
-    for (int i=0;i<4;++i){ float2 t2 = *(const float2*)(xr + i*8); v[2*i]=t2.x; v[2*i+1]=t2.y; }
-    float s1=0.f, s2=0.f;
-    #pragma unroll
-    for (int i=0;i<8;++i){ s1+=v[i]; s2+=v[i]*v[i]; }
-    for (int o=1;o<16;o<<=1){ s1 += __shfl_xor(s1,o); s2 += __shfl_xor(s2,o); }
+      if (qq<2){
+        int col = nt*16+cc; float bv = p.out_b[col];
+        #pragma unroll
+        for (int r=0;r<4;++r) *(float*)(smem + OFF_X + (qq*4+r)*XSTR + col*4) = acc[r]+bv;
+      }
+    }
+  }
+  __syncthreads();
+  {
+    const float* xr = (const float*)(smem + OFF_X + b5*XSTR + sg*16);
+    float4 v = *(const float4*)xr;
+    float s1 = v.x+v.y+v.z+v.w, s2 = v.x*v.x+v.y*v.y+v.z*v.z+v.w*v.w;
+    for (int o=1;o<32;o<<=1){ s1 += __shfl_xor(s1,o); s2 += __shfl_xor(s2,o); }
     float m = s1*0.0078125f, rs = rsqrtf(s2*0.0078125f - m*m + 1e-5f);
-    float4 o0,o1;
-    o0.x=(v[0]-m)*rs*p.out_g[pp*8+0]+p.out_bb[pp*8+0];
-    o0.y=(v[1]-m)*rs*p.out_g[pp*8+1]+p.out_bb[pp*8+1];
-    o0.z=(v[2]-m)*rs*p.out_g[pp*8+2]+p.out_bb[pp*8+2];
-    o0.w=(v[3]-m)*rs*p.out_g[pp*8+3]+p.out_bb[pp*8+3];
-    o1.x=(v[4]-m)*rs*p.out_g[pp*8+4]+p.out_bb[pp*8+4];
-    o1.y=(v[5]-m)*rs*p.out_g[pp*8+5]+p.out_bb[pp*8+5];
-    o1.z=(v[6]-m)*rs*p.out_g[pp*8+6]+p.out_bb[pp*8+6];
-    o1.w=(v[7]-m)*rs*p.out_g[pp*8+7]+p.out_bb[pp*8+7];
-    float* dst = p.outp + (size_t)(bB+b_)*128 + pp*8;
-    *(float4*)dst = o0; *(float4*)(dst+4) = o1;
+    int c0 = sg*4;
+    float4 o4;
+    o4.x = (v.x-m)*rs*p.out_g[c0+0]+p.out_bb[c0+0];
+    o4.y = (v.y-m)*rs*p.out_g[c0+1]+p.out_bb[c0+1];
+    o4.z = (v.z-m)*rs*p.out_g[c0+2]+p.out_bb[c0+2];
+    o4.w = (v.w-m)*rs*p.out_g[c0+3]+p.out_bb[c0+3];
+    *(float4*)(p.outp + (size_t)(bB+b5)*128 + sg*4) = o4;
   }
 }
 
@@ -565,51 +551,55 @@
                               hipStream_t stream){
   (void)in_sizes; (void)n_in; (void)out_size;
   char* ws = (char*)d_ws;
-  ushort* WqT  = (ushort*)(ws + 0);
-  ushort* WkT  = (ushort*)(ws + 98304);
-  ushort* WvT  = (ushort*)(ws + 196608);
-  ushort* W1T  = (ushort*)(ws + 294912);
-  ushort* WoT  = (ushort*)(ws + 688128);
-  ushort* W2T  = (ushort*)(ws + 786432);
-  ushort* egoT = (ushort*)(ws + 1179648);
-  ushort* outT = (ushort*)(ws + 1212416);
-  float*  npRec= (float*) (ws + 1245184);
-  ushort* bqF  = (ushort*)(ws + 1249792);
-  ushort* bkF  = (ushort*)(ws + 1250560);
-  ushort* bvF  = (ushort*)(ws + 1251328);
-  ushort* b1F  = (ushort*)(ws + 1252096);
-  const size_t NB_OFF  = 1255424;
-  const size_t MSK_OFF = NB_OFF + (size_t)B_*8192*2;
-  const size_t NEED    = MSK_OFF + (size_t)B_*8;
-  const bool spill = (ws_size >= NEED);
-
-  prepF<<<2688,128,0,stream>>>((const float*)d_in[20],(const float*)d_in[21],(const float*)d_in[14],(const float*)d_in[15],
-                               (const float*)d_in[22],(const float*)d_in[23],(const float*)d_in[16],(const float*)d_in[17],
-                               (const float*)d_in[24],(const float*)d_in[25],
-                               (const float*)d_in[28],(const float*)d_in[29],(const float*)d_in[18],(const float*)d_in[19],
-                               WqT,bqF,WkT,bkF,WvT,bvF,W1T,b1F);
-  prepP<<<1024,128,0,stream>>>((const float*)d_in[26],(const float*)d_in[30],(const float*)d_in[10],(const float*)d_in[32],
-                               WoT,W2T,egoT,outT);
-  prepNp<<<1,128,0,stream>>>((const float*)d_in[6],(const float*)d_in[7],(const float*)d_in[8],(const float*)d_in[9],npRec);
-
+  ushort* MT   = (ushort*)(ws + 0);
+  ushort* G    = (ushort*)(ws + 786432);
+  ushort* W1B  = (ushort*)(ws + 1572864);
+  ushort* W2B  = (ushort*)(ws + 1966080);
+  ushort* egoT = (ushort*)(ws + 2359296);
+  ushort* outT = (ushort*)(ws + 2392064);
+  float*  C0   = (float*) (ws + 2424832);
+  float*  m2   = (float*) (ws + 2437120);
+  float*  c2   = (float*) (ws + 2449408);
+  float*  bo2  = (float*) (ws + 2449536);
+  float*  b1F  = (float*) (ws + 2451072);
+  float*  bqp  = (float*) (ws + 2457216);
+  float*  bkp  = (float*) (ws + 2458752);
+  float*  bvp  = (float*) (ws + 2460288);
+  u64*    msk  = (u64*)   (ws + 2461952);
+  const size_t NB_OFF = 2527744;
+  const size_t NT_OFF = NB_OFF + (size_t)B_*16384;
+  const size_t NEED2  = NT_OFF + (size_t)B_*16384;
+  const bool mode2 = (ws_size >= NEED2);
+
+  prep_bias<<<11,256,0,stream>>>((const float*)d_in[20],(const float*)d_in[21],(const float*)d_in[15],
+                                 (const float*)d_in[22],(const float*)d_in[23],(const float*)d_in[17],
+                                 (const float*)d_in[24],(const float*)d_in[25],
+                                 (const float*)d_in[28],(const float*)d_in[29],(const float*)d_in[19],
+                                 bqp,bkp,bvp,b1F);
+  prep_bias2<<<3,256,0,stream>>>((const float*)d_in[26],(const float*)d_in[27],bvp,bo2);
+  prep_MG<<<24,256,0,stream>>>((const float*)d_in[20],(const float*)d_in[22],(const float*)d_in[24],(const float*)d_in[26],
+                               (const float*)d_in[14],(const float*)d_in[16],
+                               bqp,bkp, MT,C0,m2,c2,G);
+  prep_T<<<1664,256,0,stream>>>((const float*)d_in[28],(const float*)d_in[18],(const float*)d_in[30],
+                                (const float*)d_in[10],(const float*)d_in[32],
+                                W1B,W2B,egoT,outT);
   P p;
   p.ego=(const float*)d_in[0]; p.epos=(const float*)d_in[1]; p.evel=(const float*)d_in[2];
   p.npos=(const float*)d_in[3]; p.nvel=(const float*)d_in[4]; p.mask=(const int*)d_in[5];
   p.npW=(const float*)d_in[6]; p.npb=(const float*)d_in[7]; p.npg=(const float*)d_in[8]; p.npbb=(const float*)d_in[9];
   p.ego_b=(const float*)d_in[11]; p.ego_g=(const float*)d_in[12]; p.ego_bb=(const float*)d_in[13];
-  p.bo=(const float*)d_in[27]; p.b2=(const float*)d_in[31];
+  p.b2=(const float*)d_in[31];
   p.out_b=(const float*)d_in[33]; p.out_g=(const float*)d_in[34]; p.out_bb=(const float*)d_in[35];
-  p.npRec=npRec;
-  p.WqT=WqT; p.WkT=WkT; p.WvT=WvT; p.W1T=W1T; p.WoT=WoT; p.W2T=W2T; p.egoT=egoT; p.outT=outT;
-  p.bqF=bqF; p.bkF=bkF; p.bvF=bvF; p.b1F=b1F;
-  p.nbg = (ushort*)(ws + NB_OFF);
-  p.msk = (u64*)(ws + MSK_OFF);
+  p.C0=C0; p.m2=m2; p.c2=c2; p.bo2=bo2; p.b1F=b1F;
+  p.MT=MT; p.G=G; p.W1B=W1B; p.W2B=W2B; p.egoT=egoT; p.outT=outT;
+  p.nbg=(ushort*)(ws+NB_OFF); p.nbt=(ushort*)(ws+NT_OFF); p.msk=msk;
   p.outp=(float*)d_out;
 
-  if (spill){
-    st_nb<<<B_/2,256,0,stream>>>(p);
-    st_main<1><<<B_/16,256,0,stream>>>(p);
+  if (mode2){
+    st_nb<2><<<B_/2,256,0,stream>>>(p);
+    st_main<2><<<B_/8,256,0,stream>>>(p);
   } else {
-    st_main<0><<<B_/16,256,0,stream>>>(p);
+    st_nb<1><<<B_/2,256,0,stream>>>(p);
+    st_main<1><<<B_/8,256,0,stream>>>(p);
   }
 }
```

Result: slower. 1.265 ms (+104.4%).
